# Performance work log

Measured on AMD Instinct MI355X. Metric: run time of the kernel, lower is better.

Reference implementation:

```python
import jax, jax.numpy as jnp
import numpy as np

B, T, H, TGT = 1024, 672, 128, 96

def _lstm_cell(x, h, c, Wih, Whh, b):
    # PyTorch gate order: i, f, g, o
    z = x @ Wih.T + h @ Whh.T + b
    i, f, g, o = jnp.split(z, 4, axis=-1)
    c = jax.nn.sigmoid(f) * c + jax.nn.sigmoid(i) * jnp.tanh(g)
    h = jax.nn.sigmoid(o) * jnp.tanh(c)
    return h, c

def _run_layer(xs, Wih, Whh, b):
    # xs: [T, B, in] time-major. Returns ys [T,B,H], final (h, c).
    B_ = xs.shape[1]
    h0 = jnp.zeros((B_, Whh.shape[1]), xs.dtype)
    def step(carry, x):
        h, c = carry
        h, c = _lstm_cell(x, h, c, Wih, Whh, b)
        return (h, c), h
    (h, c), ys = jax.lax.scan(step, (h0, h0), xs)
    return ys, h, c

def setup_inputs() -> dict:
    key = jax.random.key(0)
    ks = jax.random.split(key, 24)
    s = 1.0 / np.sqrt(H)
    u = lambda k, shape: jax.random.uniform(k, shape, jnp.float32, -s, s)
    inp = {"features": jax.random.normal(ks[0], (B, T, 1), jnp.float32)}
    # encoder layer 0 (input 1), layer 1 (input H); decoder same (decoder input is 1)
    inp["enc_Wih0"] = u(ks[1], (4 * H, 1));  inp["enc_Whh0"] = u(ks[2], (4 * H, H))
    inp["enc_b0"]   = u(ks[3], (4 * H,))
    inp["enc_Wih1"] = u(ks[4], (4 * H, H)); inp["enc_Whh1"] = u(ks[5], (4 * H, H))
    inp["enc_b1"]   = u(ks[6], (4 * H,))
    inp["dec_Wih0"] = u(ks[7], (4 * H, 1));  inp["dec_Whh0"] = u(ks[8], (4 * H, H))
    inp["dec_b0"]   = u(ks[9], (4 * H,))
    inp["dec_Wih1"] = u(ks[10], (4 * H, H)); inp["dec_Whh1"] = u(ks[11], (4 * H, H))
    inp["dec_b1"]   = u(ks[12], (4 * H,))
    inp["W_out1"] = u(ks[13], (H, H)); inp["b_out1"] = u(ks[14], (H,))
    inp["W_out2"] = u(ks[15], (1, H)); inp["b_out2"] = u(ks[16], (1,))
    return inp

def reference(features, enc_Wih0, enc_Whh0, enc_b0, enc_Wih1, enc_Whh1, enc_b1,
              dec_Wih0, dec_Whh0, dec_b0, dec_Wih1, dec_Whh1, dec_b1,
              W_out1, b_out1, W_out2, b_out2):
    xs = jnp.transpose(features, (1, 0, 2))  # [T, B, 1]
    ys0, h1, c1 = _run_layer(xs, enc_Wih0, enc_Whh0, enc_b0)
    _,   h2, c2 = _run_layer(ys0, enc_Wih1, enc_Whh1, enc_b1)
    x0 = jnp.zeros((features.shape[0], 1), features.dtype)
    def dec_step(carry, _):
        h1, c1, h2, c2, x = carry
        h1, c1 = _lstm_cell(x, h1, c1, dec_Wih0, dec_Whh0, dec_b0)
        h2, c2 = _lstm_cell(h1, h2, c2, dec_Wih1, dec_Whh1, dec_b1)
        pred = jax.nn.relu(h2 @ W_out1.T + b_out1) @ W_out2.T + b_out2  # [B,1]
        return (h1, c1, h2, c2, pred), pred
    _, preds = jax.lax.scan(dec_step, (h1, c1, h2, c2, x0), None, length=TGT)
    return jnp.transpose(preds[:, :, 0], (1, 0))  # [B, TGT]
```

## Files before the change

kernel.cpp:

```cpp
#include <hip/hip_runtime.h>


#define B_    1024
#define T_    672
#define H_    128
#define G_    512
#define TGT_  96
#define NBLK_ 256

typedef __attribute__((ext_vector_type(8))) short  short8;
typedef __attribute__((ext_vector_type(4))) float  floatx4;

__device__ __forceinline__ float sigm(float x)   { return 1.f / (1.f + __expf(-x)); }
__device__ __forceinline__ float tanh_f(float x) { return 1.f - 2.f / (1.f + __expf(2.f * x)); }

__device__ __forceinline__ void step_barrier() {
    asm volatile("s_waitcnt lgkmcnt(0)" ::: "memory");
    __builtin_amdgcn_s_barrier();
}

__device__ __forceinline__ void bsplit(float a, unsigned short& h, unsigned short& l) {
    const unsigned int u  = __float_as_uint(a);
    const unsigned int hi = (u + 0x8000u) >> 16;
    const float fh = __uint_as_float(hi << 16);
    h = (unsigned short)hi;
    l = (unsigned short)(__float_as_uint(a - fh) >> 16);
}

struct PrepArgs {
    const float* dwhh0; float* pk0;
    const float* d1x; const float* d1h; float* pack;
    const float* bsrc[3];
    unsigned short* bh[3];
    unsigned short* bl[3];
};

__global__ void kPrep(PrepArgs a) {
    const int m = blockIdx.x;
    if (m == 0) {
        for (int i = threadIdx.x; i < H_ * H_; i += blockDim.x) {
            const int k = i >> 7, j4 = i & 127;
            float* p = a.pk0 + ((size_t)k * H_ + j4) * 4;
#pragma unroll
            for (int g = 0; g < 4; g++)
                p[g] = a.dwhh0[(j4 + 128 * g) * H_ + k];
        }
    } else if (m == 1) {
        for (int i = threadIdx.x; i < H_ * H_; i += blockDim.x) {
            const int k = i >> 7, j4 = i & 127;
            float* p = a.pack + ((size_t)k * H_ + j4) * 8;
#pragma unroll
            for (int g = 0; g < 4; g++) {
                p[g]     = a.d1x[(j4 + 128 * g) * H_ + k];
                p[4 + g] = a.d1h[(j4 + 128 * g) * H_ + k];
            }
        }
    } else {
        const int s = m - 2;
        const float* src = a.bsrc[s];
        unsigned short* dh = a.bh[s];
        unsigned short* dl = a.bl[s];
        for (int i = threadIdx.x; i < G_ * H_; i += blockDim.x) {
            unsigned short h, l;
            bsplit(src[i], h, l);
            dh[i] = h; dl[i] = l;
        }
    }
}

__device__ __forceinline__ void runL0(
    const float* __restrict__ feat,
    const unsigned short* __restrict__ WHh,
    const unsigned short* __restrict__ WHl,
    const float* __restrict__ wih0,
    const float* __restrict__ bias,
    unsigned short* __restrict__ Ah,
    unsigned short* __restrict__ Al,
    float* __restrict__ hS, float* __restrict__ cS,
    int t0, int CL, int bidx,
    unsigned short (*hh)[16][136], unsigned short (*hl)[16][136], float* fsh)
{
    const int tid  = threadIdx.x;
    const int lane = tid & 63;
    const int w    = tid >> 6;
    const int c15  = lane & 15;
    const int q    = lane >> 4;
    const int BG   = bidx * 16;

    short8 wh[4][4], wl[4][4];
#pragma unroll
    for (int g = 0; g < 4; g++)
#pragma unroll
        for (int kt = 0; kt < 4; kt++) {
            const size_t off = (size_t)(16 * w + 128 * g + c15) * H_ + 32 * kt + 8 * q;
            wh[g][kt] = *(const short8*)(WHh + off);
            wl[g][kt] = *(const short8*)(WHl + off);
        }

    float bz[4], wx[4];
#pragma unroll
    for (int g = 0; g < 4; g++) {
        bz[g] = bias[16 * w + 128 * g + c15];
        wx[g] = wih0[16 * w + 128 * g + c15];
    }

    for (int i = tid; i < CL * 16; i += 512)
        fsh[i] = feat[(BG + (i & 15)) * T_ + t0 + (i >> 4)];

    float cc[4], hv[4];
#pragma unroll
    for (int r = 0; r < 4; r++) { cc[r] = 0.f; hv[r] = 0.f; }
    if (t0 != 0) {
#pragma unroll
        for (int r = 0; r < 4; r++) {
            const size_t si = (size_t)(BG + 4 * q + r) * H_ + 16 * w + c15;
            cc[r] = cS[si]; hv[r] = hS[si];
        }
    }
#pragma unroll
    for (int r = 0; r < 4; r++) {
        unsigned short hi, lo; bsplit(hv[r], hi, lo);
        hh[0][4 * q + r][16 * w + c15] = hi;
        hl[0][4 * q + r][16 * w + c15] = lo;
    }
    __syncthreads();

    int pb = 0;
    unsigned int hp[4];

    for (int dt = 0; dt < CL; dt++) {
        if (dt > 0) {
#pragma unroll
            for (int r = 0; r < 4; r++) {
                const size_t ai = ((size_t)(dt - 1) * B_ + BG + 4 * q + r) * H_ + 16 * w + c15;
                Ah[ai] = (unsigned short)(hp[r] & 0xffffu);
                Al[ai] = (unsigned short)(hp[r] >> 16);
            }
        }

        floatx4 acc[4];
#pragma unroll
        for (int g = 0; g < 4; g++) acc[g] = (floatx4){0.f, 0.f, 0.f, 0.f};

#pragma unroll
        for (int kt = 0; kt < 4; kt++) {
            const short8 ahv = *(const short8*)&hh[pb][c15][32 * kt + 8 * q];
            const short8 alv = *(const short8*)&hl[pb][c15][32 * kt + 8 * q];
#pragma unroll
            for (int g = 0; g < 4; g++) {
                acc[g] = __builtin_amdgcn_mfma_f32_16x16x32_bf16(ahv, wh[g][kt], acc[g], 0, 0, 0);
                acc[g] = __builtin_amdgcn_mfma_f32_16x16x32_bf16(ahv, wl[g][kt], acc[g], 0, 0, 0);
                acc[g] = __builtin_amdgcn_mfma_f32_16x16x32_bf16(alv, wh[g][kt], acc[g], 0, 0, 0);
            }
        }

        const int nb = pb ^ 1;
#pragma unroll
        for (int r = 0; r < 4; r++) {
            const float x = fsh[dt * 16 + 4 * q + r];
            const float zi = acc[0][r] + __fmaf_rn(wx[0], x, bz[0]);
            const float zf = acc[1][r] + __fmaf_rn(wx[1], x, bz[1]);
            const float zg = acc[2][r] + __fmaf_rn(wx[2], x, bz[2]);
            const float zo = acc[3][r] + __fmaf_rn(wx[3], x, bz[3]);
            cc[r] = sigm(zf) * cc[r] + sigm(zi) * tanh_f(zg);
            const float h = sigm(zo) * tanh_f(cc[r]);
            hv[r] = h;
            unsigned short hi, lo; bsplit(h, hi, lo);
            hp[r] = (unsigned int)hi | ((unsigned int)lo << 16);
            hh[nb][4 * q + r][16 * w + c15] = hi;
            hl[nb][4 * q + r][16 * w + c15] = lo;
        }
        step_barrier();
        pb = nb;
    }

#pragma unroll
    for (int r = 0; r < 4; r++) {
        const size_t ai = ((size_t)(CL - 1) * B_ + BG + 4 * q + r) * H_ + 16 * w + c15;
        Ah[ai] = (unsigned short)(hp[r] & 0xffffu);
        Al[ai] = (unsigned short)(hp[r] >> 16);
        const size_t si = (size_t)(BG + 4 * q + r) * H_ + 16 * w + c15;
        hS[si] = hv[r]; cS[si] = cc[r];
    }
}

__device__ __forceinline__ void runL1(
    const float* __restrict__ X1,
    const unsigned short* __restrict__ WHh,
    const unsigned short* __restrict__ WHl,
    float* __restrict__ hS, float* __restrict__ cS,
    int t0, int CL, int bidx,
    unsigned short (*hh)[16][136], unsigned short (*hl)[16][136])
{
    const int tid  = threadIdx.x;
    const int lane = tid & 63;
    const int w    = tid >> 6;
    const int c15  = lane & 15;
    const int q    = lane >> 4;
    const int BG   = bidx * 16;

    short8 wh[4][4], wl[4][4];
#pragma unroll
    for (int g = 0; g < 4; g++)
#pragma unroll
        for (int kt = 0; kt < 4; kt++) {
            const size_t off = (size_t)(16 * w + 128 * g + c15) * H_ + 32 * kt + 8 * q;
            wh[g][kt] = *(const short8*)(WHh + off);
            wl[g][kt] = *(const short8*)(WHl + off);
        }

    float cc[4], hv[4];
#pragma unroll
    for (int r = 0; r < 4; r++) { cc[r] = 0.f; hv[r] = 0.f; }
    if (t0 != 0) {
#pragma unroll
        for (int r = 0; r < 4; r++) {
            const size_t si = (size_t)(BG + 4 * q + r) * H_ + 16 * w + c15;
            cc[r] = cS[si]; hv[r] = hS[si];
        }
    }
#pragma unroll
    for (int r = 0; r < 4; r++) {
        unsigned short hi, lo; bsplit(hv[r], hi, lo);
        hh[0][4 * q + r][16 * w + c15] = hi;
        hl[0][4 * q + r][16 * w + c15] = lo;
    }
    __syncthreads();

    int pb = 0;

    for (int dt = 0; dt < CL; dt++) {
        float x1v[4][4];
#pragma unroll
        for (int g = 0; g < 4; g++)
#pragma unroll
            for (int r = 0; r < 4; r++)
                x1v[g][r] = X1[((size_t)dt * B_ + BG + 4 * q + r) * G_ + 16 * w + 128 * g + c15];

        floatx4 acc[4];
#pragma unroll
        for (int g = 0; g < 4; g++) acc[g] = (floatx4){0.f, 0.f, 0.f, 0.f};

#pragma unroll
        for (int kt = 0; kt < 4; kt++) {
            const short8 ahv = *(const short8*)&hh[pb][c15][32 * kt + 8 * q];
            const short8 alv = *(const short8*)&hl[pb][c15][32 * kt + 8 * q];
#pragma unroll
            for (int g = 0; g < 4; g++) {
                acc[g] = __builtin_amdgcn_mfma_f32_16x16x32_bf16(ahv, wh[g][kt], acc[g], 0, 0, 0);
                acc[g] = __builtin_amdgcn_mfma_f32_16x16x32_bf16(ahv, wl[g][kt], acc[g], 0, 0, 0);
                acc[g] = __builtin_amdgcn_mfma_f32_16x16x32_bf16(alv, wh[g][kt], acc[g], 0, 0, 0);
            }
        }

        const int nb = pb ^ 1;
#pragma unroll
        for (int r = 0; r < 4; r++) {
            const float zi = acc[0][r] + x1v[0][r];
            const float zf = acc[1][r] + x1v[1][r];
            const float zg = acc[2][r] + x1v[2][r];
            const float zo = acc[3][r] + x1v[3][r];
            cc[r] = sigm(zf) * cc[r] + sigm(zi) * tanh_f(zg);
            const float h = sigm(zo) * tanh_f(cc[r]);
            hv[r] = h;
            unsigned short hi, lo; bsplit(h, hi, lo);
            hh[nb][4 * q + r][16 * w + c15] = hi;
            hl[nb][4 * q + r][16 * w + c15] = lo;
        }
        step_barrier();
        pb = nb;
    }

#pragma unroll
    for (int r = 0; r < 4; r++) {
        const size_t si = (size_t)(BG + 4 * q + r) * H_ + 16 * w + c15;
        hS[si] = hv[r]; cS[si] = cc[r];
    }
}

__device__ __forceinline__ void runGemm(
    const unsigned short* __restrict__ Ah,
    const unsigned short* __restrict__ Al,
    const unsigned short* __restrict__ Wh,
    const unsigned short* __restrict__ Wl,
    const float* __restrict__ bias,
    float* __restrict__ X1,
    int CL, int gbid,
    unsigned short* Bh, unsigned short* Bl)
{
    const int tid = threadIdx.x;
    const int xy  = gbid & 31;
    const int m0b = (xy >> 2) * 128;
    const int n0  = (xy & 3) * 128;

    for (int c = tid; c < 2048; c += 512) {
        const int n  = c >> 4;
        const int kb = (c & 15) << 4;
        const int sb = n * 256 + (kb ^ ((n & 7) << 4));
        *(float4*)((char*)Bh + sb) =
            *(const float4*)((const char*)Wh + (size_t)(n0 + n) * 256 + kb);
        *(float4*)((char*)Bl + sb) =
            *(const float4*)((const char*)Wl + (size_t)(n0 + n) * 256 + kb);
    }
    __syncthreads();

    const int lane = tid & 63;
    const int w    = tid >> 6;
    const int l15  = lane & 15;
    const int lq   = lane >> 4;
    const int m0   = m0b + w * 16;

    for (int dt = gbid >> 5; dt < CL; dt += 4) {
        const size_t arow = ((size_t)dt * B_ + m0 + l15) * H_;
        const unsigned short* a0h = Ah + arow;
        const unsigned short* a0l = Al + arow;

        floatx4 acc[8];
#pragma unroll
        for (int j = 0; j < 8; j++) acc[j] = (floatx4){0.f, 0.f, 0.f, 0.f};

#pragma unroll
        for (int ks = 0; ks < 4; ks++) {
            const int kk = ks * 32 + 8 * lq;
            const short8 ah = *(const short8*)(a0h + kk);
            const short8 al = *(const short8*)(a0l + kk);
            const int kbb = kk * 2;
#pragma unroll
            for (int nt = 0; nt < 8; nt++) {
                const int row = nt * 16 + l15;
                const int sb  = row * 256 + (kbb ^ ((row & 7) << 4));
                const short8 bh = *(const short8*)((const char*)Bh + sb);
                const short8 bl = *(const short8*)((const char*)Bl + sb);
                acc[nt] = __builtin_amdgcn_mfma_f32_16x16x32_bf16(ah, bh, acc[nt], 0, 0, 0);
                acc[nt] = __builtin_amdgcn_mfma_f32_16x16x32_bf16(ah, bl, acc[nt], 0, 0, 0);
                acc[nt] = __builtin_amdgcn_mfma_f32_16x16x32_bf16(al, bh, acc[nt], 0, 0, 0);
            }
        }

#pragma unroll
        for (int nt = 0; nt < 8; nt++) {
            const float bv = bias[n0 + nt * 16 + l15];
            const size_t orow = ((size_t)dt * B_ + m0 + lq * 4) * G_ + n0 + nt * 16 + l15;
#pragma unroll
            for (int r = 0; r < 4; r++)
                X1[orow + (size_t)r * G_] = acc[nt][r] + bv;
        }
    }
}

struct KFArgs {
    const float* feat;
    const unsigned short *H0h, *H0l;
    const float *wih0, *bias0;
    unsigned short *Ah0, *Al0, *Ah1, *Al1;
    float *h1S, *c1S;
    const unsigned short *Wh, *Wl;
    const float* bias1;
    float *X1a, *X1b;
    const unsigned short *H1h, *H1l;
    float *h2S, *c2S;
    int c, CL, NC;
};

__global__ __launch_bounds__(512, 2) void kF(KFArgs a) {
    __shared__ __align__(16) unsigned short hh[2][16][136];
    __shared__ __align__(16) unsigned short hl[2][16][136];
    __shared__ __align__(16) float fsh[672];
    __shared__ __align__(16) unsigned short Bh[128 * 128];
    __shared__ __align__(16) unsigned short Bl[128 * 128];

    const int c = a.c;
    if (blockIdx.x < 64) {
        if (c < a.NC) {
            unsigned short* Ah = (c & 1) ? a.Ah1 : a.Ah0;
            unsigned short* Al = (c & 1) ? a.Al1 : a.Al0;
            runL0(a.feat, a.H0h, a.H0l, a.wih0, a.bias0, Ah, Al, a.h1S, a.c1S,
                  c * a.CL, a.CL, blockIdx.x, hh, hl, fsh);
        }
    } else if (blockIdx.x < 192) {
        if (c >= 1 && c <= a.NC) {
            const int g = c - 1;
            const unsigned short* Ah = (g & 1) ? a.Ah1 : a.Ah0;
            const unsigned short* Al = (g & 1) ? a.Al1 : a.Al0;
            float* X1 = (g & 1) ? a.X1b : a.X1a;
            runGemm(Ah, Al, a.Wh, a.Wl, a.bias1, X1, a.CL, blockIdx.x - 64, Bh, Bl);
        }
    } else {
        if (c >= 2) {
            const int l = c - 2;
            const float* X1 = (l & 1) ? a.X1b : a.X1a;
            runL1(X1, a.H1h, a.H1l, a.h2S, a.c2S, l * a.CL, a.CL,
                  blockIdx.x - 192, hh, hl);
        }
    }
}

__global__ __launch_bounds__(512, 2) void kD(
    const float* __restrict__ h1S, const float* __restrict__ c1S,
    const float* __restrict__ h2S, const float* __restrict__ c2S,
    const float* __restrict__ whh0P,
    const float* __restrict__ wih0,
    const float* __restrict__ b0,
    const float* __restrict__ packD1,
    const float* __restrict__ b1,
    const float* __restrict__ wo1,
    const float* __restrict__ bo1,
    const float* __restrict__ wo2,
    const float* __restrict__ bo2,
    float* __restrict__ out)
{
    __shared__ __align__(16) float h1_sh[H_ * 4];
    __shared__ __align__(16) float h2_sh[H_ * 4];
    __shared__ __align__(16) float h2t[4][H_];
    __shared__ __align__(16) float zp[4 * 2048];
    __shared__ __align__(16) float wo1s[H_ * 132];
    __shared__ float rp[8];

    const int tid = threadIdx.x;
    const int hid = tid & 127;
    const int bb  = tid >> 7;
    const int B0  = blockIdx.x * 4;

    const float b0i = b0[hid],        b0f = b0[hid + 128];
    const float b0g = b0[hid + 256],  b0o = b0[hid + 384];
    const float wxi = wih0[hid],      wxf = wih0[hid + 128];
    const float wxg = wih0[hid + 256], wxo = wih0[hid + 384];
    const float b1i = b1[hid],        b1f = b1[hid + 128];
    const float b1g = b1[hid + 256],  b1o = b1[hid + 384];

    for (int t = tid; t < H_ * 32; t += 512) {
        const int r = t >> 5, q = t & 31;
        *(float4*)&wo1s[r * 132 + q * 4] = *(const float4*)&wo1[r * H_ + q * 4];
    }

    const float wo2v = wo2[hid];
    const float bo1j = bo1[hid];
    const float bo2v = bo2[0];

    float c1 = c1S[(B0 + bb) * H_ + hid];
    float c2 = c2S[(B0 + bb) * H_ + hid];
    h1_sh[hid * 4 + bb] = h1S[(B0 + bb) * H_ + hid];
    {
        const float h2v = h2S[(B0 + bb) * H_ + hid];
        h2_sh[hid * 4 + bb] = h2v;
        h2t[bb][hid] = h2v;
    }
    if (tid < 8) rp[tid] = -0.5f * bo2v;
    __syncthreads();

    const float* hb1 = h1_sh + bb * 128;
    const float* hb2 = h2_sh + bb * 128;
    const float* pk  = packD1 + ((size_t)bb * 32 * H_ + hid) * 8;
    const float* pw0 = whh0P + (size_t)bb * 32 * 512 + hid * 4;

    for (int s = 0; s < TGT_; s++) {
        {
            float a[4][4] = {};
#pragma unroll 8
            for (int k = 0; k < 32; k++) {
                const float4 wv = *(const float4*)&pw0[(size_t)k * 512];
                const float4 h4 = *(const float4*)&hb1[k * 4];
                a[0][0] = __fmaf_rn(h4.x, wv.x, a[0][0]);
                a[0][1] = __fmaf_rn(h4.y, wv.x, a[0][1]);
                a[0][2] = __fmaf_rn(h4.z, wv.x, a[0][2]);
                a[0][3] = __fmaf_rn(h4.w, wv.x, a[0][3]);
                a[1][0] = __fmaf_rn(h4.x, wv.y, a[1][0]);
                a[1][1] = __fmaf_rn(h4.y, wv.y, a[1][1]);
                a[1][2] = __fmaf_rn(h4.z, wv.y, a[1][2]);
                a[1][3] = __fmaf_rn(h4.w, wv.y, a[1][3]);
                a[2][0] = __fmaf_rn(h4.x, wv.z, a[2][0]);
                a[2][1] = __fmaf_rn(h4.y, wv.z, a[2][1]);
                a[2][2] = __fmaf_rn(h4.z, wv.z, a[2][2]);
                a[2][3] = __fmaf_rn(h4.w, wv.z, a[2][3]);
                a[3][0] = __fmaf_rn(h4.x, wv.w, a[3][0]);
                a[3][1] = __fmaf_rn(h4.y, wv.w, a[3][1]);
                a[3][2] = __fmaf_rn(h4.z, wv.w, a[3][2]);
                a[3][3] = __fmaf_rn(h4.w, wv.w, a[3][3]);
            }
#pragma unroll
            for (int g = 0; g < 4; g++)
#pragma unroll
                for (int b = 0; b < 4; b++)
                    zp[bb * 2048 + b * 512 + hid + 128 * g] = a[g][b];
        }
        {
            float hacc = bo1j;
#pragma unroll
            for (int q = 0; q < 32; q++) {
                const float4 hq = *(const float4*)&h2t[bb][q * 4];
                const float4 wq = *(const float4*)&wo1s[hid * 132 + q * 4];
                hacc = __fmaf_rn(hq.x, wq.x, hacc);
                hacc = __fmaf_rn(hq.y, wq.y, hacc);
                hacc = __fmaf_rn(hq.z, wq.z, hacc);
                hacc = __fmaf_rn(hq.w, wq.w, hacc);
            }
            float p = fmaxf(hacc, 0.f) * wo2v;
            p += __shfl_down(p, 32); p += __shfl_down(p, 16); p += __shfl_down(p, 8);
            p += __shfl_down(p, 4);  p += __shfl_down(p, 2);  p += __shfl_down(p, 1);
            if ((tid & 63) == 0) rp[tid >> 6] = p;
        }
        __syncthreads();

        {
            const float pred = rp[2 * bb] + rp[2 * bb + 1] + bo2v;
            if (hid == 0 && s > 0) out[(B0 + bb) * TGT_ + (s - 1)] = pred;
            const int base = bb * 512 + hid;
            float zi = __fmaf_rn(wxi, pred, b0i);
            float zf = __fmaf_rn(wxf, pred, b0f);
            float zg = __fmaf_rn(wxg, pred, b0g);
            float zo = __fmaf_rn(wxo, pred, b0o);
#pragma unroll
            for (int q = 0; q < 4; q++) {
                zi += zp[q * 2048 + base];
                zf += zp[q * 2048 + base + 128];
                zg += zp[q * 2048 + base + 256];
                zo += zp[q * 2048 + base + 384];
            }
            c1 = sigm(zf) * c1 + sigm(zi) * tanh_f(zg);
            h1_sh[hid * 4 + bb] = sigm(zo) * tanh_f(c1);
        }
        __syncthreads();

        {
            float d[4][4] = {};
#pragma unroll 8
            for (int k = 0; k < 32; k++) {
                const float4 wi = *(const float4*)&pk[(size_t)k * 1024];
                const float4 wh = *(const float4*)&pk[(size_t)k * 1024 + 4];
                const float4 p1 = *(const float4*)&hb1[k * 4];
                const float4 p2 = *(const float4*)&hb2[k * 4];
                d[0][0] = __fmaf_rn(p1.x, wi.x, __fmaf_rn(p2.x, wh.x, d[0][0]));
                d[0][1] = __fmaf_rn(p1.y, wi.x, __fmaf_rn(p2.y, wh.x, d[0][1]));
                d[0][2] = __fmaf_rn(p1.z, wi.x, __fmaf_rn(p2.z, wh.x, d[0][2]));
                d[0][3] = __fmaf_rn(p1.w, wi.x, __fmaf_rn(p2.w, wh.x, d[0][3]));
                d[1][0] = __fmaf_rn(p1.x, wi.y, __fmaf_rn(p2.x, wh.y, d[1][0]));
                d[1][1] = __fmaf_rn(p1.y, wi.y, __fmaf_rn(p2.y, wh.y, d[1][1]));
                d[1][2] = __fmaf_rn(p1.z, wi.y, __fmaf_rn(p2.z, wh.y, d[1][2]));
                d[1][3] = __fmaf_rn(p1.w, wi.y, __fmaf_rn(p2.w, wh.y, d[1][3]));
                d[2][0] = __fmaf_rn(p1.x, wi.z, __fmaf_rn(p2.x, wh.z, d[2][0]));
                d[2][1] = __fmaf_rn(p1.y, wi.z, __fmaf_rn(p2.y, wh.z, d[2][1]));
                d[2][2] = __fmaf_rn(p1.z, wi.z, __fmaf_rn(p2.z, wh.z, d[2][2]));
                d[2][3] = __fmaf_rn(p1.w, wi.z, __fmaf_rn(p2.w, wh.z, d[2][3]));
                d[3][0] = __fmaf_rn(p1.x, wi.w, __fmaf_rn(p2.x, wh.w, d[3][0]));
                d[3][1] = __fmaf_rn(p1.y, wi.w, __fmaf_rn(p2.y, wh.w, d[3][1]));
                d[3][2] = __fmaf_rn(p1.z, wi.w, __fmaf_rn(p2.z, wh.w, d[3][2]));
                d[3][3] = __fmaf_rn(p1.w, wi.w, __fmaf_rn(p2.w, wh.w, d[3][3]));
            }
#pragma unroll
            for (int g = 0; g < 4; g++)
#pragma unroll
                for (int b = 0; b < 4; b++)
                    zp[bb * 2048 + b * 512 + hid + 128 * g] = d[g][b];
        }
        __syncthreads();

        {
            const int base = bb * 512 + hid;
            float zi = b1i, zf = b1f, zg = b1g, zo = b1o;
#pragma unroll
            for (int q = 0; q < 4; q++) {
                zi += zp[q * 2048 + base];
                zf += zp[q * 2048 + base + 128];
                zg += zp[q * 2048 + base + 256];
                zo += zp[q * 2048 + base + 384];
            }
            c2 = sigm(zf) * c2 + sigm(zi) * tanh_f(zg);
            const float h2v = sigm(zo) * tanh_f(c2);
            h2_sh[hid * 4 + bb] = h2v;
            h2t[bb][hid] = h2v;
        }
        __syncthreads();
    }

    {
        float hacc = bo1j;
#pragma unroll
        for (int q = 0; q < 32; q++) {
            const float4 hq = *(const float4*)&h2t[bb][q * 4];
            const float4 wq = *(const float4*)&wo1s[hid * 132 + q * 4];
            hacc = __fmaf_rn(hq.x, wq.x, hacc);
            hacc = __fmaf_rn(hq.y, wq.y, hacc);
            hacc = __fmaf_rn(hq.z, wq.z, hacc);
            hacc = __fmaf_rn(hq.w, wq.w, hacc);
        }
        float p = fmaxf(hacc, 0.f) * wo2v;
        p += __shfl_down(p, 32); p += __shfl_down(p, 16); p += __shfl_down(p, 8);
        p += __shfl_down(p, 4);  p += __shfl_down(p, 2);  p += __shfl_down(p, 1);
        if ((tid & 63) == 0) rp[tid >> 6] = p;
    }
    __syncthreads();
    if (tid < 4)
        out[(B0 + tid) * TGT_ + (TGT_ - 1)] = rp[2 * tid] + rp[2 * tid + 1] + bo2v;
}

extern "C" void kernel_launch(void* const* d_in, const int* in_sizes, int n_in,
                              void* d_out, int out_size, void* d_ws, size_t ws_size,
                              hipStream_t stream) {
    const float* feat  = (const float*)d_in[0];
    const float* eWih0 = (const float*)d_in[1];
    const float* eWhh0 = (const float*)d_in[2];
    const float* eB0   = (const float*)d_in[3];
    const float* eWih1 = (const float*)d_in[4];
    const float* eWhh1 = (const float*)d_in[5];
    const float* eB1   = (const float*)d_in[6];
    const float* dWih0 = (const float*)d_in[7];
    const float* dWhh0 = (const float*)d_in[8];
    const float* dB0   = (const float*)d_in[9];
    const float* dWih1 = (const float*)d_in[10];
    const float* dWhh1 = (const float*)d_in[11];
    const float* dB1   = (const float*)d_in[12];
    const float* Wo1   = (const float*)d_in[13];
    const float* bo1   = (const float*)d_in[14];
    const float* Wo2   = (const float*)d_in[15];
    const float* bo2   = (const float*)d_in[16];

    const size_t SZ_BH = (size_t)B_ * H_;
    const size_t SZ_W  = (size_t)G_ * H_;
    const size_t fixed_f = 4 * SZ_BH + 6 * SZ_W + 64;

    static const int cands[] = {42, 32, 28, 24, 21, 16, 14, 12, 8, 7, 6, 4, 3, 2, 1};
    int CL = 1;
    for (int ci = 0; ci < 15; ci++) {
        const size_t need = (fixed_f + 2 * (size_t)cands[ci] * B_ * (H_ + G_)) * 4;
        if (need <= ws_size) { CL = cands[ci]; break; }
    }
    const int NC = T_ / CL;

    float* ws = (float*)d_ws;
    unsigned short* Ah0 = (unsigned short*)ws;
    unsigned short* Al0 = Ah0 + (size_t)CL * B_ * H_;
    unsigned short* Ah1 = Al0 + (size_t)CL * B_ * H_;
    unsigned short* Al1 = Ah1 + (size_t)CL * B_ * H_;
    float* X1a   = ws + 2 * (size_t)CL * B_ * H_;
    float* X1b   = X1a + (size_t)CL * B_ * G_;
    float* h1S   = X1b + (size_t)CL * B_ * G_;
    float* c1S   = h1S + SZ_BH;
    float* h2S   = c1S + SZ_BH;
    float* c2S   = h2S + SZ_BH;
    float* pk0   = c2S + SZ_BH;
    float* wtD1p = pk0 + SZ_W;
    unsigned short* Wh  = (unsigned short*)(wtD1p + 2 * SZ_W);
    unsigned short* Wl  = Wh + SZ_W;
    unsigned short* H0h = Wl + SZ_W;
    unsigned short* H0l = H0h + SZ_W;
    unsigned short* H1h = H0l + SZ_W;
    unsigned short* H1l = H1h + SZ_W;

    PrepArgs pa;
    pa.dwhh0 = dWhh0; pa.pk0 = pk0;
    pa.d1x = dWih1; pa.d1h = dWhh1; pa.pack = wtD1p;
    pa.bsrc[0] = eWih1; pa.bh[0] = Wh;  pa.bl[0] = Wl;
    pa.bsrc[1] = eWhh0; pa.bh[1] = H0h; pa.bl[1] = H0l;
    pa.bsrc[2] = eWhh1; pa.bh[2] = H1h; pa.bl[2] = H1l;
    kPrep<<<5, 256, 0, stream>>>(pa);

    KFArgs fa;
    fa.feat = feat; fa.H0h = H0h; fa.H0l = H0l; fa.wih0 = eWih0; fa.bias0 = eB0;
    fa.Ah0 = Ah0; fa.Al0 = Al0; fa.Ah1 = Ah1; fa.Al1 = Al1;
    fa.h1S = h1S; fa.c1S = c1S;
    fa.Wh = Wh; fa.Wl = Wl; fa.bias1 = eB1;
    fa.X1a = X1a; fa.X1b = X1b;
    fa.H1h = H1h; fa.H1l = H1l; fa.h2S = h2S; fa.c2S = c2S;
    fa.CL = CL; fa.NC = NC;

    for (int c = 0; c <= NC + 1; c++) {
        fa.c = c;
        kF<<<256, 512, 0, stream>>>(fa);
    }
    kD<<<NBLK_, 512, 0, stream>>>(h1S, c1S, h2S, c2S,
                                  pk0, dWih0, dB0,
                                  wtD1p, dB1,
                                  Wo1, bo1, Wo2, bo2,
                                  (float*)d_out);
}
```

Measured before the change: 2.838 ms.

## Give each decoder thread a full K reduction, removing cross-warp partial sums

The decoder kernel changes how work is split across the 512 threads. Before, the hidden-dimension reduction was split four ways across warps, with partial sums exchanged through a large shared buffer. Now each thread handles one batch row and runs the full 128-long reduction itself, and h2 is double-buffered, which removes one barrier and the shared-memory partial-sum round trip per step. In exchange each thread reads four times as much weight data from global memory/cache, and the weight packing layout is reinterpreted, so the result depends on the pack order matching.

```diff
diff --git a/kernel.cpp b/kernel.cpp
--- a/kernel.cpp
+++ b/kernel.cpp
@@ -395,7 +395,7 @@
     }
 }
 
-__global__ __launch_bounds__(512, 2) void kD(
+__global__ __launch_bounds__(512, 2) void kD4(
     const float* __restrict__ h1S, const float* __restrict__ c1S,
     const float* __restrict__ h2S, const float* __restrict__ c2S,
     const float* __restrict__ whh0P,
@@ -409,10 +409,8 @@
     const float* __restrict__ bo2,
     float* __restrict__ out)
 {
-    __shared__ __align__(16) float h1_sh[H_ * 4];
-    __shared__ __align__(16) float h2_sh[H_ * 4];
-    __shared__ __align__(16) float h2t[4][H_];
-    __shared__ __align__(16) float zp[4 * 2048];
+    __shared__ __align__(16) float h1sh[4][128];
+    __shared__ __align__(16) float h2sh[2][4][128];
     __shared__ __align__(16) float wo1s[H_ * 132];
     __shared__ float rp[8];
 
@@ -439,55 +437,42 @@
 
     float c1 = c1S[(B0 + bb) * H_ + hid];
     float c2 = c2S[(B0 + bb) * H_ + hid];
-    h1_sh[hid * 4 + bb] = h1S[(B0 + bb) * H_ + hid];
-    {
-        const float h2v = h2S[(B0 + bb) * H_ + hid];
-        h2_sh[hid * 4 + bb] = h2v;
-        h2t[bb][hid] = h2v;
-    }
+    h1sh[bb][hid]    = h1S[(B0 + bb) * H_ + hid];
+    h2sh[0][bb][hid] = h2S[(B0 + bb) * H_ + hid];
     if (tid < 8) rp[tid] = -0.5f * bo2v;
     __syncthreads();
 
-    const float* hb1 = h1_sh + bb * 128;
-    const float* hb2 = h2_sh + bb * 128;
-    const float* pk  = packD1 + ((size_t)bb * 32 * H_ + hid) * 8;
-    const float* pw0 = whh0P + (size_t)bb * 32 * 512 + hid * 4;
+    const float* pw0 = whh0P + hid * 4;
+    const float* pk  = packD1 + hid * 8;
+    int pb = 0;
 
     for (int s = 0; s < TGT_; s++) {
+        float a0 = 0.f, a1 = 0.f, a2 = 0.f, a3 = 0.f;
         {
-            float a[4][4] = {};
-#pragma unroll 8
-            for (int k = 0; k < 32; k++) {
-                const float4 wv = *(const float4*)&pw0[(size_t)k * 512];
-                const float4 h4 = *(const float4*)&hb1[k * 4];
-                a[0][0] = __fmaf_rn(h4.x, wv.x, a[0][0]);
-                a[0][1] = __fmaf_rn(h4.y, wv.x, a[0][1]);
-                a[0][2] = __fmaf_rn(h4.z, wv.x, a[0][2]);
-                a[0][3] = __fmaf_rn(h4.w, wv.x, a[0][3]);
-                a[1][0] = __fmaf_rn(h4.x, wv.y, a[1][0]);
-                a[1][1] = __fmaf_rn(h4.y, wv.y, a[1][1]);
-                a[1][2] = __fmaf_rn(h4.z, wv.y, a[1][2]);
-                a[1][3] = __fmaf_rn(h4.w, wv.y, a[1][3]);
-                a[2][0] = __fmaf_rn(h4.x, wv.z, a[2][0]);
-                a[2][1] = __fmaf_rn(h4.y, wv.z, a[2][1]);
-                a[2][2] = __fmaf_rn(h4.z, wv.z, a[2][2]);
-                a[2][3] = __fmaf_rn(h4.w, wv.z, a[2][3]);
-                a[3][0] = __fmaf_rn(h4.x, wv.w, a[3][0]);
-                a[3][1] = __fmaf_rn(h4.y, wv.w, a[3][1]);
-                a[3][2] = __fmaf_rn(h4.z, wv.w, a[3][2]);
-                a[3][3] = __fmaf_rn(h4.w, wv.w, a[3][3]);
-            }
-#pragma unroll
-            for (int g = 0; g < 4; g++)
-#pragma unroll
-                for (int b = 0; b < 4; b++)
-                    zp[bb * 2048 + b * 512 + hid + 128 * g] = a[g][b];
+            const float* h1p = h1sh[bb];
+#pragma unroll 4
+            for (int kk = 0; kk < 32; kk++) {
+                const float4 hq = *(const float4*)&h1p[kk * 4];
+                const float4 w0 = *(const float4*)&pw0[(size_t)(kk * 4 + 0) * 512];
+                const float4 w1 = *(const float4*)&pw0[(size_t)(kk * 4 + 1) * 512];
+                const float4 w2 = *(const float4*)&pw0[(size_t)(kk * 4 + 2) * 512];
+                const float4 w3 = *(const float4*)&pw0[(size_t)(kk * 4 + 3) * 512];
+                a0 = __fmaf_rn(hq.x, w0.x, a0); a1 = __fmaf_rn(hq.x, w0.y, a1);
+                a2 = __fmaf_rn(hq.x, w0.z, a2); a3 = __fmaf_rn(hq.x, w0.w, a3);
+                a0 = __fmaf_rn(hq.y, w1.x, a0); a1 = __fmaf_rn(hq.y, w1.y, a1);
+                a2 = __fmaf_rn(hq.y, w1.z, a2); a3 = __fmaf_rn(hq.y, w1.w, a3);
+                a0 = __fmaf_rn(hq.z, w2.x, a0); a1 = __fmaf_rn(hq.z, w2.y, a1);
+                a2 = __fmaf_rn(hq.z, w2.z, a2); a3 = __fmaf_rn(hq.z, w2.w, a3);
+                a0 = __fmaf_rn(hq.w, w3.x, a0); a1 = __fmaf_rn(hq.w, w3.y, a1);
+                a2 = __fmaf_rn(hq.w, w3.z, a2); a3 = __fmaf_rn(hq.w, w3.w, a3);
+            }
         }
         {
             float hacc = bo1j;
-#pragma unroll
+            const float* h2p = h2sh[pb][bb];
+#pragma unroll 4
             for (int q = 0; q < 32; q++) {
-                const float4 hq = *(const float4*)&h2t[bb][q * 4];
+                const float4 hq = *(const float4*)&h2p[q * 4];
                 const float4 wq = *(const float4*)&wo1s[hid * 132 + q * 4];
                 hacc = __fmaf_rn(hq.x, wq.x, hacc);
                 hacc = __fmaf_rn(hq.y, wq.y, hacc);
@@ -504,79 +489,73 @@
         {
             const float pred = rp[2 * bb] + rp[2 * bb + 1] + bo2v;
             if (hid == 0 && s > 0) out[(B0 + bb) * TGT_ + (s - 1)] = pred;
-            const int base = bb * 512 + hid;
-            float zi = __fmaf_rn(wxi, pred, b0i);
-            float zf = __fmaf_rn(wxf, pred, b0f);
-            float zg = __fmaf_rn(wxg, pred, b0g);
-            float zo = __fmaf_rn(wxo, pred, b0o);
-#pragma unroll
-            for (int q = 0; q < 4; q++) {
-                zi += zp[q * 2048 + base];
-                zf += zp[q * 2048 + base + 128];
-                zg += zp[q * 2048 + base + 256];
-                zo += zp[q * 2048 + base + 384];
-            }
+            const float zi = a0 + __fmaf_rn(wxi, pred, b0i);
+            const float zf = a1 + __fmaf_rn(wxf, pred, b0f);
+            const float zg = a2 + __fmaf_rn(wxg, pred, b0g);
+            const float zo = a3 + __fmaf_rn(wxo, pred, b0o);
             c1 = sigm(zf) * c1 + sigm(zi) * tanh_f(zg);
-            h1_sh[hid * 4 + bb] = sigm(zo) * tanh_f(c1);
+            h1sh[bb][hid] = sigm(zo) * tanh_f(c1);
         }
         __syncthreads();
 
         {
-            float d[4][4] = {};
-#pragma unroll 8
-            for (int k = 0; k < 32; k++) {
-                const float4 wi = *(const float4*)&pk[(size_t)k * 1024];
-                const float4 wh = *(const float4*)&pk[(size_t)k * 1024 + 4];
-                const float4 p1 = *(const float4*)&hb1[k * 4];
-                const float4 p2 = *(const float4*)&hb2[k * 4];
-                d[0][0] = __fmaf_rn(p1.x, wi.x, __fmaf_rn(p2.x, wh.x, d[0][0]));
-                d[0][1] = __fmaf_rn(p1.y, wi.x, __fmaf_rn(p2.y, wh.x, d[0][1]));
-                d[0][2] = __fmaf_rn(p1.z, wi.x, __fmaf_rn(p2.z, wh.x, d[0][2]));
-                d[0][3] = __fmaf_rn(p1.w, wi.x, __fmaf_rn(p2.w, wh.x, d[0][3]));
-                d[1][0] = __fmaf_rn(p1.x, wi.y, __fmaf_rn(p2.x, wh.y, d[1][0]));
-                d[1][1] = __fmaf_rn(p1.y, wi.y, __fmaf_rn(p2.y, wh.y, d[1][1]));
-                d[1][2] = __fmaf_rn(p1.z, wi.y, __fmaf_rn(p2.z, wh.y, d[1][2]));
-                d[1][3] = __fmaf_rn(p1.w, wi.y, __fmaf_rn(p2.w, wh.y, d[1][3]));
-                d[2][0] = __fmaf_rn(p1.x, wi.z, __fmaf_rn(p2.x, wh.z, d[2][0]));
-                d[2][1] = __fmaf_rn(p1.y, wi.z, __fmaf_rn(p2.y, wh.z, d[2][1]));
-                d[2][2] = __fmaf_rn(p1.z, wi.z, __fmaf_rn(p2.z, wh.z, d[2][2]));
-                d[2][3] = __fmaf_rn(p1.w, wi.z, __fmaf_rn(p2.w, wh.z, d[2][3]));
-                d[3][0] = __fmaf_rn(p1.x, wi.w, __fmaf_rn(p2.x, wh.w, d[3][0]));
-                d[3][1] = __fmaf_rn(p1.y, wi.w, __fmaf_rn(p2.y, wh.w, d[3][1]));
-                d[3][2] = __fmaf_rn(p1.z, wi.w, __fmaf_rn(p2.z, wh.w, d[3][2]));
-                d[3][3] = __fmaf_rn(p1.w, wi.w, __fmaf_rn(p2.w, wh.w, d[3][3]));
-            }
-#pragma unroll
-            for (int g = 0; g < 4; g++)
-#pragma unroll
-                for (int b = 0; b < 4; b++)
-                    zp[bb * 2048 + b * 512 + hid + 128 * g] = d[g][b];
+            float d0 = 0.f, d1 = 0.f, d2 = 0.f, d3 = 0.f;
+            const float* h1p = h1sh[bb];
+            const float* h2p = h2sh[pb][bb];
+#pragma unroll 2
+            for (int kk = 0; kk < 32; kk++) {
+                const float4 p1 = *(const float4*)&h1p[kk * 4];
+                const float4 p2 = *(const float4*)&h2p[kk * 4];
+                {
+                    const float4 wi = *(const float4*)&pk[(size_t)(kk * 4 + 0) * 1024];
+                    const float4 wh = *(const float4*)&pk[(size_t)(kk * 4 + 0) * 1024 + 4];
+                    d0 = __fmaf_rn(p1.x, wi.x, __fmaf_rn(p2.x, wh.x, d0));
+                    d1 = __fmaf_rn(p1.x, wi.y, __fmaf_rn(p2.x, wh.y, d1));
+                    d2 = __fmaf_rn(p1.x, wi.z, __fmaf_rn(p2.x, wh.z, d2));
+                    d3 = __fmaf_rn(p1.x, wi.w, __fmaf_rn(p2.x, wh.w, d3));
+                }
+                {
+                    const float4 wi = *(const float4*)&pk[(size_t)(kk * 4 + 1) * 1024];
+                    const float4 wh = *(const float4*)&pk[(size_t)(kk * 4 + 1) * 1024 + 4];
+                    d0 = __fmaf_rn(p1.y, wi.x, __fmaf_rn(p2.y, wh.x, d0));
+                    d1 = __fmaf_rn(p1.y, wi.y, __fmaf_rn(p2.y, wh.y, d1));
+                    d2 = __fmaf_rn(p1.y, wi.z, __fmaf_rn(p2.y, wh.z, d2));
+                    d3 = __fmaf_rn(p1.y, wi.w, __fmaf_rn(p2.y, wh.w, d3));
+                }
+                {
+                    const float4 wi = *(const float4*)&pk[(size_t)(kk * 4 + 2) * 1024];
+                    const float4 wh = *(const float4*)&pk[(size_t)(kk * 4 + 2) * 1024 + 4];
+                    d0 = __fmaf_rn(p1.z, wi.x, __fmaf_rn(p2.z, wh.x, d0));
+                    d1 = __fmaf_rn(p1.z, wi.y, __fmaf_rn(p2.z, wh.y, d1));
+                    d2 = __fmaf_rn(p1.z, wi.z, __fmaf_rn(p2.z, wh.z, d2));
+                    d3 = __fmaf_rn(p1.z, wi.w, __fmaf_rn(p2.z, wh.w, d3));
+                }
+                {
+                    const float4 wi = *(const float4*)&pk[(size_t)(kk * 4 + 3) * 1024];
+                    const float4 wh = *(const float4*)&pk[(size_t)(kk * 4 + 3) * 1024 + 4];
+                    d0 = __fmaf_rn(p1.w, wi.x, __fmaf_rn(p2.w, wh.x, d0));
+                    d1 = __fmaf_rn(p1.w, wi.y, __fmaf_rn(p2.w, wh.y, d1));
+                    d2 = __fmaf_rn(p1.w, wi.z, __fmaf_rn(p2.w, wh.z, d2));
+                    d3 = __fmaf_rn(p1.w, wi.w, __fmaf_rn(p2.w, wh.w, d3));
+                }
+            }
+            const float zi = d0 + b1i;
+            const float zf = d1 + b1f;
+            const float zg = d2 + b1g;
+            const float zo = d3 + b1o;
+            c2 = sigm(zf) * c2 + sigm(zi) * tanh_f(zg);
+            h2sh[pb ^ 1][bb][hid] = sigm(zo) * tanh_f(c2);
         }
         __syncthreads();
-
-        {
-            const int base = bb * 512 + hid;
-            float zi = b1i, zf = b1f, zg = b1g, zo = b1o;
-#pragma unroll
-            for (int q = 0; q < 4; q++) {
-                zi += zp[q * 2048 + base];
-                zf += zp[q * 2048 + base + 128];
-                zg += zp[q * 2048 + base + 256];
-                zo += zp[q * 2048 + base + 384];
-            }
-            c2 = sigm(zf) * c2 + sigm(zi) * tanh_f(zg);
-            const float h2v = sigm(zo) * tanh_f(c2);
-            h2_sh[hid * 4 + bb] = h2v;
-            h2t[bb][hid] = h2v;
-        }
-        __syncthreads();
+        pb ^= 1;
     }
 
     {
         float hacc = bo1j;
-#pragma unroll
+        const float* h2p = h2sh[pb][bb];
+#pragma unroll 4
         for (int q = 0; q < 32; q++) {
-            const float4 hq = *(const float4*)&h2t[bb][q * 4];
+            const float4 hq = *(const float4*)&h2p[q * 4];
             const float4 wq = *(const float4*)&wo1s[hid * 132 + q * 4];
             hacc = __fmaf_rn(hq.x, wq.x, hacc);
             hacc = __fmaf_rn(hq.y, wq.y, hacc);
@@ -667,9 +646,9 @@
         fa.c = c;
         kF<<<256, 512, 0, stream>>>(fa);
     }
-    kD<<<NBLK_, 512, 0, stream>>>(h1S, c1S, h2S, c2S,
-                                  pk0, dWih0, dB0,
-                                  wtD1p, dB1,
-                                  Wo1, bo1, Wo2, bo2,
-                                  (float*)d_out);
-}
+    kD4<<<NBLK_, 512, 0, stream>>>(h1S, c1S, h2S, c2S,
+                                   pk0, dWih0, dB0,
+                                   wtD1p, dB1,
+                                   Wo1, bo1, Wo2, bo2,
+                                   (float*)d_out);
+}
```

New measurement: 4.233 ms. 49.1% more time.
